# Optimization experiments

Measured on AMD Instinct MI355X. Metric: run time of the kernel, lower is better.

The kernel has to match this reference:

```python
import jax, jax.numpy as jnp
import numpy as np

N_NODES = 100000
N_EDGES = 1600000
IN_FEATS = 256
OUT_FEATS = 64


def setup_inputs() -> dict:
    key = jax.random.key(0)
    k1, k2, k3, k4, k5 = jax.random.split(key, 5)
    feat = jax.random.normal(k1, (N_NODES, IN_FEATS), dtype=jnp.float32)
    W = jax.random.normal(k2, (IN_FEATS, OUT_FEATS), dtype=jnp.float32)
    ew = jax.random.uniform(k3, (N_EDGES,), dtype=jnp.float32)
    src = jax.random.randint(k4, (N_EDGES,), 0, N_NODES, dtype=jnp.int64)
    dst = jax.random.randint(k5, (N_EDGES,), 0, N_NODES, dtype=jnp.int64)
    return {"feat": feat, "W": W, "ew": ew, "src": src, "dst": dst}


def reference(feat, W, ew, src, dst):
    # h = feat @ W  (node-level projection)
    h = feat @ W                              # [N, out]
    # src_mul_edge: m_e = h[src_e] * w_e ; fn.sum: h_v = sum_{e: dst_e=v} m_e
    msg = h[src] * ew[:, None]                # [E, out]
    agg = jax.ops.segment_sum(msg, dst, num_segments=N_NODES)  # [N, out]
    return jax.nn.relu(agg)
```

## Files before the change

kernel.cpp:

```cpp
#include <hip/hip_runtime.h>

#define IN_F 256
#define OUT_F 64
#define LOGSB 8
#define SBNODES 256
#define MAXSB 1024

typedef __bf16 bf16x8 __attribute__((ext_vector_type(8)));
typedef float f32x4 __attribute__((ext_vector_type(4)));

__global__ __launch_bounds__(64) void wfrag_kernel(const float* __restrict__ W,
                                                   __bf16* __restrict__ wfrag,
                                                   int* __restrict__ bcnt, int nsb) {
    const int st = blockIdx.x;
    const int l = threadIdx.x;
    if (st == 0)
        for (int i = l; i <= nsb; i += 64) bcnt[i] = 0;
    const int s = st >> 2, t = st & 3;
    const int n = t * 16 + (l & 15);
    const int k0 = s * 32 + (l >> 4) * 8;
    bf16x8 f;
#pragma unroll
    for (int j = 0; j < 8; ++j)
        f[j] = (__bf16)W[(k0 + j) * OUT_F + n];
    *(bf16x8*)(wfrag + (size_t)(st * 64 + l) * 8) = f;
}

__global__ __launch_bounds__(256) void gemm_mfma_kernel(const float* __restrict__ feat,
                                                        const __bf16* __restrict__ wfrag,
                                                        __bf16* __restrict__ h, int N) {
    const int tid = threadIdx.x;
    const int wv = tid >> 6;
    const int l = tid & 63;
    const int m0 = blockIdx.x * 64 + wv * 16;
    const int q = l >> 4;
    const int row = min(m0 + (l & 15), N - 1);

    const float* __restrict__ arow = feat + (size_t)row * IN_F + q * 8;
    const bf16x8* __restrict__ wf = (const bf16x8*)wfrag;

    f32x4 acc0 = {0.f, 0.f, 0.f, 0.f};
    f32x4 acc1 = {0.f, 0.f, 0.f, 0.f};
    f32x4 acc2 = {0.f, 0.f, 0.f, 0.f};
    f32x4 acc3 = {0.f, 0.f, 0.f, 0.f};

#pragma unroll
    for (int s = 0; s < 8; ++s) {
        float4 fa0 = *(const float4*)(arow + s * 32);
        float4 fa1 = *(const float4*)(arow + s * 32 + 4);
        bf16x8 a;
        a[0] = (__bf16)fa0.x; a[1] = (__bf16)fa0.y;
        a[2] = (__bf16)fa0.z; a[3] = (__bf16)fa0.w;
        a[4] = (__bf16)fa1.x; a[5] = (__bf16)fa1.y;
        a[6] = (__bf16)fa1.z; a[7] = (__bf16)fa1.w;
        bf16x8 b0 = wf[(s * 4 + 0) * 64 + l];
        bf16x8 b1 = wf[(s * 4 + 1) * 64 + l];
        bf16x8 b2 = wf[(s * 4 + 2) * 64 + l];
        bf16x8 b3 = wf[(s * 4 + 3) * 64 + l];
        acc0 = __builtin_amdgcn_mfma_f32_16x16x32_bf16(a, b0, acc0, 0, 0, 0);
        acc1 = __builtin_amdgcn_mfma_f32_16x16x32_bf16(a, b1, acc1, 0, 0, 0);
        acc2 = __builtin_amdgcn_mfma_f32_16x16x32_bf16(a, b2, acc2, 0, 0, 0);
        acc3 = __builtin_amdgcn_mfma_f32_16x16x32_bf16(a, b3, acc3, 0, 0, 0);
    }

    const int colb = l & 15;
#pragma unroll
    for (int r = 0; r < 4; ++r) {
        int ro = m0 + q * 4 + r;
        if (ro < N) {
            __bf16* hp = h + (size_t)ro * OUT_F + colb;
            hp[0]  = (__bf16)acc0[r];
            hp[16] = (__bf16)acc1[r];
            hp[32] = (__bf16)acc2[r];
            hp[48] = (__bf16)acc3[r];
        }
    }
}

__global__ __launch_bounds__(256) void sbhist_kernel(const int* __restrict__ dst,
                                                     int* __restrict__ bcnt, int E, int nsb) {
    __shared__ int hist[MAXSB];
    for (int i = threadIdx.x; i < nsb; i += 256) hist[i] = 0;
    __syncthreads();
    const int stride = gridDim.x * 1024;
    for (int base = (blockIdx.x * 256 + threadIdx.x) * 4; base < E; base += stride) {
        if (base + 4 <= E) {
            int4 d4 = *(const int4*)(dst + base);
            atomicAdd(&hist[d4.x >> LOGSB], 1);
            atomicAdd(&hist[d4.y >> LOGSB], 1);
            atomicAdd(&hist[d4.z >> LOGSB], 1);
            atomicAdd(&hist[d4.w >> LOGSB], 1);
        } else {
            for (int e = base; e < E; ++e) atomicAdd(&hist[dst[e] >> LOGSB], 1);
        }
    }
    __syncthreads();
    for (int i = threadIdx.x; i < nsb; i += 256)
        if (hist[i]) atomicAdd(&bcnt[i], hist[i]);
}

__global__ __launch_bounds__(1024) void sbscan_kernel(const int* __restrict__ bcnt,
                                                      int* __restrict__ sbbase,
                                                      int* __restrict__ sbcur,
                                                      int* __restrict__ noff,
                                                      int nsb, int N, int E) {
    __shared__ int s[1024];
    const int t = threadIdx.x;
    int v = (t < nsb) ? bcnt[t] : 0;
    s[t] = v;
    __syncthreads();
    for (int o = 1; o < 1024; o <<= 1) {
        int x = (t >= o) ? s[t - o] : 0;
        __syncthreads();
        s[t] += x;
        __syncthreads();
    }
    if (t < nsb) {
        int ex = s[t] - v;
        sbbase[t] = ex;
        sbcur[t] = ex;
    }
    if (t == 0) {
        sbbase[nsb] = E;
        noff[N] = E;
    }
}

__global__ __launch_bounds__(1024) void sbscatter_kernel(const int* __restrict__ src,
                                                         const int* __restrict__ dst,
                                                         const float* __restrict__ ew,
                                                         int* __restrict__ sbcur,
                                                         int2* __restrict__ payload,
                                                         int E, int nsb) {
    __shared__ int cnt[MAXSB];
    __shared__ int basearr[MAXSB];
    const int t = threadIdx.x;
    for (int i = t; i < nsb; i += 1024) cnt[i] = 0;
    __syncthreads();

    const int base = (blockIdx.x * 1024 + t) * 4;
    int dd[4] = {0, 0, 0, 0}, ss[4] = {0, 0, 0, 0};
    float ww[4] = {0.f, 0.f, 0.f, 0.f};
    int nv = 0;
    if (base + 4 <= E) {
        int4 d4 = *(const int4*)(dst + base);
        int4 s4 = *(const int4*)(src + base);
        float4 w4 = *(const float4*)(ew + base);
        dd[0] = d4.x; dd[1] = d4.y; dd[2] = d4.z; dd[3] = d4.w;
        ss[0] = s4.x; ss[1] = s4.y; ss[2] = s4.z; ss[3] = s4.w;
        ww[0] = w4.x; ww[1] = w4.y; ww[2] = w4.z; ww[3] = w4.w;
        nv = 4;
    } else if (base < E) {
        nv = E - base;
#pragma unroll 4
        for (int j = 0; j < 4; ++j)
            if (j < nv) { dd[j] = dst[base + j]; ss[j] = src[base + j]; ww[j] = ew[base + j]; }
    }

    int idx[4];
#pragma unroll 4
    for (int j = 0; j < 4; ++j)
        if (j < nv) idx[j] = atomicAdd(&cnt[dd[j] >> LOGSB], 1);
    __syncthreads();

    for (int i = t; i < nsb; i += 1024)
        if (cnt[i]) basearr[i] = atomicAdd(&sbcur[i], cnt[i]);
    __syncthreads();

#pragma unroll 4
    for (int j = 0; j < 4; ++j)
        if (j < nv) {
            int pos = basearr[dd[j] >> LOGSB] + idx[j];
            payload[pos] = make_int2(ss[j] | ((dd[j] & (SBNODES - 1)) << 24),
                                     __float_as_int(ww[j]));
        }
}

__global__ __launch_bounds__(256) void fsort_kernel(const int2* __restrict__ payload,
                                                    int2* __restrict__ payload2,
                                                    const int* __restrict__ sbbase,
                                                    int* __restrict__ noff, int N) {
    __shared__ int cnt[SBNODES];
    __shared__ int off[SBNODES + 1];
    __shared__ int tick[SBNODES];
    const int t = threadIdx.x;
    const int b = sbbase[blockIdx.x];
    const int e = sbbase[blockIdx.x + 1];
    const int m = e - b;

    cnt[t] = 0;
    __syncthreads();
    for (int i = t; i < m; i += 256)
        atomicAdd(&cnt[((unsigned)payload[b + i].x) >> 24], 1);
    __syncthreads();

    if (t == 0) off[0] = 0;
    off[t + 1] = cnt[t];
    __syncthreads();
    for (int o = 1; o < SBNODES; o <<= 1) {
        int v = (t >= o) ? off[t + 1 - o] : 0;
        __syncthreads();
        off[t + 1] += v;
        __syncthreads();
    }

    const int g = (blockIdx.x << LOGSB) + t;
    if (g < N) noff[g] = b + off[t];
    tick[t] = 0;
    __syncthreads();

    for (int i = t; i < m; i += 256) {
        int2 p = payload[b + i];
        int ld = ((unsigned)p.x) >> 24;
        int pos = b + off[ld] + atomicAdd(&tick[ld], 1);
        payload2[pos] = make_int2(p.x & 0xFFFFFF, p.y);
    }
}

#define EDGE8(PBASE, A0A, A0B, A1A, A1B, A2A, A2B, A3A, A3B)                    \
    {                                                                           \
        int2 p0 = (PBASE)[0];                                                   \
        int2 p1 = (PBASE)[1];                                                   \
        int2 p2 = (PBASE)[2];                                                   \
        int2 p3 = (PBASE)[3];                                                   \
        int2 p4 = (PBASE)[4];                                                   \
        int2 p5 = (PBASE)[5];                                                   \
        int2 p6 = (PBASE)[6];                                                   \
        int2 p7 = (PBASE)[7];                                                   \
        unsigned v0 = h32[(size_t)p0.x * 32 + j];                               \
        unsigned v1 = h32[(size_t)p1.x * 32 + j];                               \
        unsigned v2 = h32[(size_t)p2.x * 32 + j];                               \
        unsigned v3 = h32[(size_t)p3.x * 32 + j];                               \
        unsigned v4 = h32[(size_t)p4.x * 32 + j];                               \
        unsigned v5 = h32[(size_t)p5.x * 32 + j];                               \
        unsigned v6 = h32[(size_t)p6.x * 32 + j];                               \
        unsigned v7 = h32[(size_t)p7.x * 32 + j];                               \
        float w0 = __int_as_float(p0.y), w1 = __int_as_float(p1.y);             \
        float w2 = __int_as_float(p2.y), w3 = __int_as_float(p3.y);             \
        float w4 = __int_as_float(p4.y), w5 = __int_as_float(p5.y);             \
        float w6 = __int_as_float(p6.y), w7 = __int_as_float(p7.y);             \
        A0A = fmaf(__uint_as_float(v0 << 16), w0, A0A);                         \
        A0B = fmaf(__uint_as_float(v0 & 0xFFFF0000u), w0, A0B);                 \
        A1A = fmaf(__uint_as_float(v1 << 16), w1, A1A);                         \
        A1B = fmaf(__uint_as_float(v1 & 0xFFFF0000u), w1, A1B);                 \
        A2A = fmaf(__uint_as_float(v2 << 16), w2, A2A);                         \
        A2B = fmaf(__uint_as_float(v2 & 0xFFFF0000u), w2, A2B);                 \
        A3A = fmaf(__uint_as_float(v3 << 16), w3, A3A);                         \
        A3B = fmaf(__uint_as_float(v3 & 0xFFFF0000u), w3, A3B);                 \
        A0A = fmaf(__uint_as_float(v4 << 16), w4, A0A);                         \
        A0B = fmaf(__uint_as_float(v4 & 0xFFFF0000u), w4, A0B);                 \
        A1A = fmaf(__uint_as_float(v5 << 16), w5, A1A);                         \
        A1B = fmaf(__uint_as_float(v5 & 0xFFFF0000u), w5, A1B);                 \
        A2A = fmaf(__uint_as_float(v6 << 16), w6, A2A);                         \
        A2B = fmaf(__uint_as_float(v6 & 0xFFFF0000u), w6, A2B);                 \
        A3A = fmaf(__uint_as_float(v7 << 16), w7, A3A);                         \
        A3B = fmaf(__uint_as_float(v7 & 0xFFFF0000u), w7, A3B);                 \
    }

__global__ __launch_bounds__(256) void bgather_kernel(const __bf16* __restrict__ h,
                                                      const int2* __restrict__ payload2,
                                                      const int* __restrict__ noff,
                                                      float* __restrict__ out, int N) {
    const int t = threadIdx.x;
    const int hw = t >> 5;
    const int j = t & 31;
    const unsigned* __restrict__ h32 = (const unsigned*)h;
    const int g0 = blockIdx.x * 32;

#pragma unroll 1
    for (int k = 0; k < 4; ++k) {
        const int g = g0 + hw + k * 8;
        if (g >= N) continue;
        int i = noff[g];
        const int eE = noff[g + 1];
        float a0A = 0.f, a0B = 0.f, a1A = 0.f, a1B = 0.f;
        float a2A = 0.f, a2B = 0.f, a3A = 0.f, a3B = 0.f;
        float b0A = 0.f, b0B = 0.f, b1A = 0.f, b1B = 0.f;
        float b2A = 0.f, b2B = 0.f, b3A = 0.f, b3B = 0.f;
#pragma unroll 1
        for (; i + 16 <= eE; i += 16) {
            EDGE8(payload2 + i, a0A, a0B, a1A, a1B, a2A, a2B, a3A, a3B)
            EDGE8(payload2 + i + 8, b0A, b0B, b1A, b1B, b2A, b2B, b3A, b3B)
        }
        if (i + 8 <= eE) {
            EDGE8(payload2 + i, a0A, a0B, a1A, a1B, a2A, a2B, a3A, a3B)
            i += 8;
        }
        for (; i + 2 <= eE; i += 2) {
            int2 p0 = payload2[i + 0];
            int2 p1 = payload2[i + 1];
            unsigned v0 = h32[(size_t)p0.x * 32 + j];
            unsigned v1 = h32[(size_t)p1.x * 32 + j];
            float w0 = __int_as_float(p0.y), w1 = __int_as_float(p1.y);
            a0A = fmaf(__uint_as_float(v0 << 16), w0, a0A);
            a0B = fmaf(__uint_as_float(v0 & 0xFFFF0000u), w0, a0B);
            a1A = fmaf(__uint_as_float(v1 << 16), w1, a1A);
            a1B = fmaf(__uint_as_float(v1 & 0xFFFF0000u), w1, a1B);
        }
        if (i < eE) {
            int2 p0 = payload2[i];
            unsigned v0 = h32[(size_t)p0.x * 32 + j];
            float w0 = __int_as_float(p0.y);
            a0A = fmaf(__uint_as_float(v0 << 16), w0, a0A);
            a0B = fmaf(__uint_as_float(v0 & 0xFFFF0000u), w0, a0B);
        }
        float2 v;
        v.x = fmaxf(((a0A + a1A) + (a2A + a3A)) + ((b0A + b1A) + (b2A + b3A)), 0.f);
        v.y = fmaxf(((a0B + a1B) + (a2B + a3B)) + ((b0B + b1B) + (b2B + b3B)), 0.f);
        *(float2*)(out + (size_t)g * OUT_F + 2 * j) = v;
    }
}

extern "C" void kernel_launch(void* const* d_in, const int* in_sizes, int n_in,
                              void* d_out, int out_size, void* d_ws, size_t ws_size,
                              hipStream_t stream) {
    const float* feat = (const float*)d_in[0];
    const float* W    = (const float*)d_in[1];
    const float* ew   = (const float*)d_in[2];
    const int*   src  = (const int*)d_in[3];
    const int*   dst  = (const int*)d_in[4];
    float* out = (float*)d_out;

    const int N = in_sizes[0] / IN_F;
    const int E = in_sizes[2];
    const int nsb = (N + SBNODES - 1) >> LOGSB;

    char* ws = (char*)d_ws;
    int2*   payload  = (int2*)ws;   ws += (size_t)E * 8;
    int2*   payload2 = (int2*)ws;   ws += (size_t)E * 8;
    __bf16* h        = (__bf16*)ws; ws += (size_t)N * OUT_F * 2;
    __bf16* wfrag    = (__bf16*)ws; ws += 32 * 64 * 8 * 2;
    int*    bcnt     = (int*)ws;    ws += (MAXSB + 1) * 4;
    int*    sbbase   = (int*)ws;    ws += (MAXSB + 1) * 4;
    int*    sbcur    = (int*)ws;    ws += MAXSB * 4;
    int*    noff     = (int*)ws;

    hipLaunchKernelGGL(wfrag_kernel, dim3(32), dim3(64), 0, stream, W, wfrag, bcnt, nsb);
    hipLaunchKernelGGL(sbhist_kernel, dim3(512), dim3(256), 0, stream, dst, bcnt, E, nsb);
    hipLaunchKernelGGL(sbscan_kernel, dim3(1), dim3(1024), 0, stream, bcnt, sbbase, sbcur, noff, nsb, N, E);
    hipLaunchKernelGGL(sbscatter_kernel, dim3((E + 4095) / 4096), dim3(1024), 0, stream,
                       src, dst, ew, sbcur, payload, E, nsb);
    hipLaunchKernelGGL(fsort_kernel, dim3(nsb), dim3(256), 0, stream, payload, payload2, sbbase, noff, N);
    hipLaunchKernelGGL(gemm_mfma_kernel, dim3((N + 63) / 64), dim3(256), 0, stream, feat, wfrag, h, N);
    hipLaunchKernelGGL(bgather_kernel, dim3((N + 31) / 32), dim3(256), 0, stream, h, payload2, noff, out, N);
}
```

Measured before the change: 128.7 us.

## Fuse GEMM with histogram, fold scan into scatter and fsort, cache edges

Merges the MFMA projection and the destination-bucket histogram into one launch, with separate block ranges for each. The standalone single-block scan kernel is removed: each scatter block recomputes the superblock prefix sum from bcnt, and fsort rebuilds its base offset with a block reduction. fsort also keeps up to 4096 edges in registers so the payload is read once instead of twice. This cuts two launches and a serial scan step, at the cost of redundant scan work in every block and higher register pressure in fsort.

```diff
diff --git a/kernel.cpp b/kernel.cpp
--- a/kernel.cpp
+++ b/kernel.cpp
@@ -11,11 +11,14 @@
 
 __global__ __launch_bounds__(64) void wfrag_kernel(const float* __restrict__ W,
                                                    __bf16* __restrict__ wfrag,
-                                                   int* __restrict__ bcnt, int nsb) {
+                                                   int* __restrict__ bcnt,
+                                                   int* __restrict__ sbcur, int nsb) {
     const int st = blockIdx.x;
     const int l = threadIdx.x;
     if (st == 0)
         for (int i = l; i <= nsb; i += 64) bcnt[i] = 0;
+    if (st == 1)
+        for (int i = l; i < nsb; i += 64) sbcur[i] = 0;
     const int s = st >> 2, t = st & 3;
     const int n = t * 16 + (l & 15);
     const int k0 = s * 32 + (l >> 4) * 8;
@@ -26,115 +29,106 @@
     *(bf16x8*)(wfrag + (size_t)(st * 64 + l) * 8) = f;
 }
 
-__global__ __launch_bounds__(256) void gemm_mfma_kernel(const float* __restrict__ feat,
-                                                        const __bf16* __restrict__ wfrag,
-                                                        __bf16* __restrict__ h, int N) {
-    const int tid = threadIdx.x;
-    const int wv = tid >> 6;
-    const int l = tid & 63;
-    const int m0 = blockIdx.x * 64 + wv * 16;
-    const int q = l >> 4;
-    const int row = min(m0 + (l & 15), N - 1);
-
-    const float* __restrict__ arow = feat + (size_t)row * IN_F + q * 8;
-    const bf16x8* __restrict__ wf = (const bf16x8*)wfrag;
-
-    f32x4 acc0 = {0.f, 0.f, 0.f, 0.f};
-    f32x4 acc1 = {0.f, 0.f, 0.f, 0.f};
-    f32x4 acc2 = {0.f, 0.f, 0.f, 0.f};
-    f32x4 acc3 = {0.f, 0.f, 0.f, 0.f};
-
-#pragma unroll
-    for (int s = 0; s < 8; ++s) {
-        float4 fa0 = *(const float4*)(arow + s * 32);
-        float4 fa1 = *(const float4*)(arow + s * 32 + 4);
-        bf16x8 a;
-        a[0] = (__bf16)fa0.x; a[1] = (__bf16)fa0.y;
-        a[2] = (__bf16)fa0.z; a[3] = (__bf16)fa0.w;
-        a[4] = (__bf16)fa1.x; a[5] = (__bf16)fa1.y;
-        a[6] = (__bf16)fa1.z; a[7] = (__bf16)fa1.w;
-        bf16x8 b0 = wf[(s * 4 + 0) * 64 + l];
-        bf16x8 b1 = wf[(s * 4 + 1) * 64 + l];
-        bf16x8 b2 = wf[(s * 4 + 2) * 64 + l];
-        bf16x8 b3 = wf[(s * 4 + 3) * 64 + l];
-        acc0 = __builtin_amdgcn_mfma_f32_16x16x32_bf16(a, b0, acc0, 0, 0, 0);
-        acc1 = __builtin_amdgcn_mfma_f32_16x16x32_bf16(a, b1, acc1, 0, 0, 0);
-        acc2 = __builtin_amdgcn_mfma_f32_16x16x32_bf16(a, b2, acc2, 0, 0, 0);
-        acc3 = __builtin_amdgcn_mfma_f32_16x16x32_bf16(a, b3, acc3, 0, 0, 0);
-    }
-
-    const int colb = l & 15;
-#pragma unroll
-    for (int r = 0; r < 4; ++r) {
-        int ro = m0 + q * 4 + r;
-        if (ro < N) {
-            __bf16* hp = h + (size_t)ro * OUT_F + colb;
-            hp[0]  = (__bf16)acc0[r];
-            hp[16] = (__bf16)acc1[r];
-            hp[32] = (__bf16)acc2[r];
-            hp[48] = (__bf16)acc3[r];
-        }
-    }
-}
-
-__global__ __launch_bounds__(256) void sbhist_kernel(const int* __restrict__ dst,
-                                                     int* __restrict__ bcnt, int E, int nsb) {
-    __shared__ int hist[MAXSB];
-    for (int i = threadIdx.x; i < nsb; i += 256) hist[i] = 0;
-    __syncthreads();
-    const int stride = gridDim.x * 1024;
-    for (int base = (blockIdx.x * 256 + threadIdx.x) * 4; base < E; base += stride) {
-        if (base + 4 <= E) {
-            int4 d4 = *(const int4*)(dst + base);
-            atomicAdd(&hist[d4.x >> LOGSB], 1);
-            atomicAdd(&hist[d4.y >> LOGSB], 1);
-            atomicAdd(&hist[d4.z >> LOGSB], 1);
-            atomicAdd(&hist[d4.w >> LOGSB], 1);
-        } else {
-            for (int e = base; e < E; ++e) atomicAdd(&hist[dst[e] >> LOGSB], 1);
-        }
-    }
-    __syncthreads();
-    for (int i = threadIdx.x; i < nsb; i += 256)
-        if (hist[i]) atomicAdd(&bcnt[i], hist[i]);
-}
-
-__global__ __launch_bounds__(1024) void sbscan_kernel(const int* __restrict__ bcnt,
-                                                      int* __restrict__ sbbase,
-                                                      int* __restrict__ sbcur,
-                                                      int* __restrict__ noff,
-                                                      int nsb, int N, int E) {
-    __shared__ int s[1024];
-    const int t = threadIdx.x;
-    int v = (t < nsb) ? bcnt[t] : 0;
-    s[t] = v;
-    __syncthreads();
-    for (int o = 1; o < 1024; o <<= 1) {
-        int x = (t >= o) ? s[t - o] : 0;
-        __syncthreads();
-        s[t] += x;
-        __syncthreads();
-    }
-    if (t < nsb) {
-        int ex = s[t] - v;
-        sbbase[t] = ex;
-        sbcur[t] = ex;
-    }
-    if (t == 0) {
-        sbbase[nsb] = E;
-        noff[N] = E;
+__global__ __launch_bounds__(256) void gemmhist_kernel(const float* __restrict__ feat,
+                                                       const __bf16* __restrict__ wfrag,
+                                                       __bf16* __restrict__ h, int N,
+                                                       const int* __restrict__ dst,
+                                                       int* __restrict__ bcnt, int E, int nsb,
+                                                       int gemmBlocks) {
+    __shared__ int histo[MAXSB];
+    if ((int)blockIdx.x < gemmBlocks) {
+        const int tid = threadIdx.x;
+        const int wv = tid >> 6;
+        const int l = tid & 63;
+        const int m0 = blockIdx.x * 64 + wv * 16;
+        const int q = l >> 4;
+        const int row = min(m0 + (l & 15), N - 1);
+
+        const float* __restrict__ arow = feat + (size_t)row * IN_F + q * 8;
+        const bf16x8* __restrict__ wf = (const bf16x8*)wfrag;
+
+        f32x4 acc0 = {0.f, 0.f, 0.f, 0.f};
+        f32x4 acc1 = {0.f, 0.f, 0.f, 0.f};
+        f32x4 acc2 = {0.f, 0.f, 0.f, 0.f};
+        f32x4 acc3 = {0.f, 0.f, 0.f, 0.f};
+
+#pragma unroll
+        for (int s = 0; s < 8; ++s) {
+            float4 fa0 = *(const float4*)(arow + s * 32);
+            float4 fa1 = *(const float4*)(arow + s * 32 + 4);
+            bf16x8 a;
+            a[0] = (__bf16)fa0.x; a[1] = (__bf16)fa0.y;
+            a[2] = (__bf16)fa0.z; a[3] = (__bf16)fa0.w;
+            a[4] = (__bf16)fa1.x; a[5] = (__bf16)fa1.y;
+            a[6] = (__bf16)fa1.z; a[7] = (__bf16)fa1.w;
+            bf16x8 b0 = wf[(s * 4 + 0) * 64 + l];
+            bf16x8 b1 = wf[(s * 4 + 1) * 64 + l];
+            bf16x8 b2 = wf[(s * 4 + 2) * 64 + l];
+            bf16x8 b3 = wf[(s * 4 + 3) * 64 + l];
+            acc0 = __builtin_amdgcn_mfma_f32_16x16x32_bf16(a, b0, acc0, 0, 0, 0);
+            acc1 = __builtin_amdgcn_mfma_f32_16x16x32_bf16(a, b1, acc1, 0, 0, 0);
+            acc2 = __builtin_amdgcn_mfma_f32_16x16x32_bf16(a, b2, acc2, 0, 0, 0);
+            acc3 = __builtin_amdgcn_mfma_f32_16x16x32_bf16(a, b3, acc3, 0, 0, 0);
+        }
+
+        const int colb = l & 15;
+#pragma unroll
+        for (int r = 0; r < 4; ++r) {
+            int ro = m0 + q * 4 + r;
+            if (ro < N) {
+                __bf16* hp = h + (size_t)ro * OUT_F + colb;
+                hp[0]  = (__bf16)acc0[r];
+                hp[16] = (__bf16)acc1[r];
+                hp[32] = (__bf16)acc2[r];
+                hp[48] = (__bf16)acc3[r];
+            }
+        }
+    } else {
+        const int hb = blockIdx.x - gemmBlocks;
+        const int nhb = gridDim.x - gemmBlocks;
+        for (int i = threadIdx.x; i < nsb; i += 256) histo[i] = 0;
+        __syncthreads();
+        const int stride = nhb * 1024;
+        for (int base = (hb * 256 + threadIdx.x) * 4; base < E; base += stride) {
+            if (base + 4 <= E) {
+                int4 d4 = *(const int4*)(dst + base);
+                atomicAdd(&histo[d4.x >> LOGSB], 1);
+                atomicAdd(&histo[d4.y >> LOGSB], 1);
+                atomicAdd(&histo[d4.z >> LOGSB], 1);
+                atomicAdd(&histo[d4.w >> LOGSB], 1);
+            } else {
+                for (int e = base; e < E; ++e) atomicAdd(&histo[dst[e] >> LOGSB], 1);
+            }
+        }
+        __syncthreads();
+        for (int i = threadIdx.x; i < nsb; i += 256)
+            if (histo[i]) atomicAdd(&bcnt[i], histo[i]);
     }
 }
 
 __global__ __launch_bounds__(1024) void sbscatter_kernel(const int* __restrict__ src,
                                                          const int* __restrict__ dst,
                                                          const float* __restrict__ ew,
+                                                         const int* __restrict__ bcnt,
                                                          int* __restrict__ sbcur,
                                                          int2* __restrict__ payload,
                                                          int E, int nsb) {
+    __shared__ int s[1024];
+    __shared__ int sbb[MAXSB];
     __shared__ int cnt[MAXSB];
     __shared__ int basearr[MAXSB];
     const int t = threadIdx.x;
+
+    int v = (t < nsb) ? bcnt[t] : 0;
+    s[t] = v;
+    __syncthreads();
+    for (int o = 1; o < 1024; o <<= 1) {
+        int x = (t >= o) ? s[t - o] : 0;
+        __syncthreads();
+        s[t] += x;
+        __syncthreads();
+    }
+    if (t < nsb) sbb[t] = s[t] - v;
     for (int i = t; i < nsb; i += 1024) cnt[i] = 0;
     __syncthreads();
 
@@ -164,7 +158,7 @@
     __syncthreads();
 
     for (int i = t; i < nsb; i += 1024)
-        if (cnt[i]) basearr[i] = atomicAdd(&sbcur[i], cnt[i]);
+        if (cnt[i]) basearr[i] = sbb[i] + atomicAdd(&sbcur[i], cnt[i]);
     __syncthreads();
 
 #pragma unroll 4
@@ -178,19 +172,43 @@
 
 __global__ __launch_bounds__(256) void fsort_kernel(const int2* __restrict__ payload,
                                                     int2* __restrict__ payload2,
-                                                    const int* __restrict__ sbbase,
-                                                    int* __restrict__ noff, int N) {
+                                                    const int* __restrict__ bcnt,
+                                                    int* __restrict__ noff,
+                                                    int N, int E, int nsb) {
+    __shared__ int red[256];
     __shared__ int cnt[SBNODES];
     __shared__ int off[SBNODES + 1];
     __shared__ int tick[SBNODES];
     const int t = threadIdx.x;
-    const int b = sbbase[blockIdx.x];
-    const int e = sbbase[blockIdx.x + 1];
-    const int m = e - b;
+    const int bid = blockIdx.x;
+
+    int partial = 0;
+    for (int i = t; i < bid; i += 256) partial += bcnt[i];
+    red[t] = partial;
+    __syncthreads();
+    for (int o = 128; o > 0; o >>= 1) {
+        if (t < o) red[t] += red[t + o];
+        __syncthreads();
+    }
+    const int b = red[0];
+    const int m = bcnt[bid];
+    const int mlim = min(m, 4096);
+
+    int2 ed[16];
+#pragma unroll
+    for (int k = 0; k < 16; ++k) {
+        int i = t + k * 256;
+        if (i < mlim) ed[k] = payload[b + i];
+    }
 
     cnt[t] = 0;
     __syncthreads();
-    for (int i = t; i < m; i += 256)
+#pragma unroll
+    for (int k = 0; k < 16; ++k) {
+        int i = t + k * 256;
+        if (i < mlim) atomicAdd(&cnt[((unsigned)ed[k].x) >> 24], 1);
+    }
+    for (int i = 4096 + t; i < m; i += 256)
         atomicAdd(&cnt[((unsigned)payload[b + i].x) >> 24], 1);
     __syncthreads();
 
@@ -198,18 +216,29 @@
     off[t + 1] = cnt[t];
     __syncthreads();
     for (int o = 1; o < SBNODES; o <<= 1) {
-        int v = (t >= o) ? off[t + 1 - o] : 0;
-        __syncthreads();
-        off[t + 1] += v;
-        __syncthreads();
-    }
-
-    const int g = (blockIdx.x << LOGSB) + t;
+        int v2 = (t >= o) ? off[t + 1 - o] : 0;
+        __syncthreads();
+        off[t + 1] += v2;
+        __syncthreads();
+    }
+
+    const int g = (bid << LOGSB) + t;
     if (g < N) noff[g] = b + off[t];
+    if (bid == 0 && t == 0) noff[N] = E;
     tick[t] = 0;
     __syncthreads();
 
-    for (int i = t; i < m; i += 256) {
+#pragma unroll
+    for (int k = 0; k < 16; ++k) {
+        int i = t + k * 256;
+        if (i < mlim) {
+            int2 p = ed[k];
+            int ld = ((unsigned)p.x) >> 24;
+            int pos = b + off[ld] + atomicAdd(&tick[ld], 1);
+            payload2[pos] = make_int2(p.x & 0xFFFFFF, p.y);
+        }
+    }
+    for (int i = 4096 + t; i < m; i += 256) {
         int2 p = payload[b + i];
         int ld = ((unsigned)p.x) >> 24;
         int pos = b + off[ld] + atomicAdd(&tick[ld], 1);
@@ -331,16 +360,18 @@
     __bf16* h        = (__bf16*)ws; ws += (size_t)N * OUT_F * 2;
     __bf16* wfrag    = (__bf16*)ws; ws += 32 * 64 * 8 * 2;
     int*    bcnt     = (int*)ws;    ws += (MAXSB + 1) * 4;
-    int*    sbbase   = (int*)ws;    ws += (MAXSB + 1) * 4;
     int*    sbcur    = (int*)ws;    ws += MAXSB * 4;
     int*    noff     = (int*)ws;
 
-    hipLaunchKernelGGL(wfrag_kernel, dim3(32), dim3(64), 0, stream, W, wfrag, bcnt, nsb);
-    hipLaunchKernelGGL(sbhist_kernel, dim3(512), dim3(256), 0, stream, dst, bcnt, E, nsb);
-    hipLaunchKernelGGL(sbscan_kernel, dim3(1), dim3(1024), 0, stream, bcnt, sbbase, sbcur, noff, nsb, N, E);
+    const int gemmBlocks = (N + 63) / 64;
+
+    hipLaunchKernelGGL(wfrag_kernel, dim3(32), dim3(64), 0, stream, W, wfrag, bcnt, sbcur, nsb);
+    hipLaunchKernelGGL(gemmhist_kernel, dim3(gemmBlocks + 512), dim3(256), 0, stream,
+                       feat, wfrag, h, N, dst, bcnt, E, nsb, gemmBlocks);
     hipLaunchKernelGGL(sbscatter_kernel, dim3((E + 4095) / 4096), dim3(1024), 0, stream,
-                       src, dst, ew, sbcur, payload, E, nsb);
-    hipLaunchKernelGGL(fsort_kernel, dim3(nsb), dim3(256), 0, stream, payload, payload2, sbbase, noff, N);
-    hipLaunchKernelGGL(gemm_mfma_kernel, dim3((N + 63) / 64), dim3(256), 0, stream, feat, wfrag, h, N);
-    hipLaunchKernelGGL(bgather_kernel, dim3((N + 31) / 32), dim3(256), 0, stream, h, payload2, noff, out, N);
-}
+                       src, dst, ew, bcnt, sbcur, payload, E, nsb);
+    hipLaunchKernelGGL(fsort_kernel, dim3(nsb), dim3(256), 0, stream,
+                       payload, payload2, bcnt, noff, N, E, nsb);
+    hipLaunchKernelGGL(bgather_kernel, dim3((N + 31) / 32), dim3(256), 0, stream,
+                       h, payload2, noff, out, N);
+}
```

After: 119.6 us. 7.1% less time.
